# Kernel tuning notes

Hardware: AMD Instinct MI355X
Metric: run time of the kernel (lower is better)

Reference implementation:

```python
import jax, jax.numpy as jnp
import numpy as np

DILATED_K = 3  # init kwarg dilated_parameter_k -> 2**k = 8


def setup_inputs() -> dict:
    key = jax.random.key(0)
    k1, k2, k3, k4 = jax.random.split(key, 4)
    B, H, R, F = 16, 8, 400, 256
    A = jax.random.uniform(k1, (B, H, R, R), dtype=jnp.float32)
    feats = jax.random.normal(k2, (B, H, R, F), dtype=jnp.float32)
    # Linear(features, features) params (torch layout: weight [out, in], bias [out])
    lim = 1.0 / np.sqrt(F)
    W = jax.random.uniform(k3, (F, F), dtype=jnp.float32, minval=-lim, maxval=lim)
    b = jax.random.uniform(k4, (F,), dtype=jnp.float32, minval=-lim, maxval=lim)
    return {"Adjancy_Matrix": A, "features": feats, "W": W, "b": b}


def reference(Adjancy_Matrix, features, W, b):
    # Deterministic reference: takes the prob < 0.8 (dilated) branch of the
    # original module (the other branch is pure random dropout of the mask).
    two_k = 2 ** DILATED_K  # 8
    # torch.sort(A, descending=True, dim=3).indices == argsort of -A along last dim
    idx = jnp.argsort(-Adjancy_Matrix, axis=3)  # [B,H,R,R] int32
    # mask = 1 where sorted column index is 0 or in {2^k, ..., 2^k+4}
    mask = (idx == 0) | ((idx >= two_k) & (idx <= two_k + 4))
    R = Adjancy_Matrix.shape[2]
    mask = mask | jnp.eye(R, dtype=bool)  # add identity per (b, h), clamp >=1 -> 1
    masked_A = Adjancy_Matrix * mask.astype(Adjancy_Matrix.dtype)
    agg = jnp.einsum('bhij,bhjf->bhif', masked_A, features)  # [B,H,R,F]
    out = jax.nn.relu(agg @ W.T + b)
    return out + features
```

## Files before the change

### kernel.cpp

```cpp
#include <hip/hip_runtime.h>

typedef unsigned short u16;
typedef unsigned int   u32;
typedef __bf16 bf16x8 __attribute__((ext_vector_type(8)));
typedef float  f32x4  __attribute__((ext_vector_type(4)));
typedef u32    u32x4  __attribute__((ext_vector_type(4)));
typedef u16    u16x4  __attribute__((ext_vector_type(4)));
typedef u16    u16x8v __attribute__((ext_vector_type(8)));

#define R_DIM 400
#define F_DIM 256
#define M_TOT 51200
#define INVALID 0xFFFFFFFFu

__device__ __forceinline__ u16 f2bf(float f) {
    union { float f; u32 i; } x; x.f = f;
    u32 r = x.i + 0x7FFFu + ((x.i >> 16) & 1u);
    return (u16)(r >> 16);
}

__global__ __launch_bounds__(256) void wprep_f32(const float* __restrict__ W,
                                                 u16* __restrict__ Wf) {
    int g  = blockIdx.x * 256 + threadIdx.x;
    int ks = g >> 10;
    int T  = (g >> 6) & 15;
    int L  = g & 63;
    int n  = T * 16 + (L & 15);
    int k  = ks * 32 + (L >> 4) * 8;
    const float* wp = W + (size_t)n * F_DIM + k;
    float4 lo = *(const float4*)wp;
    float4 hi = *(const float4*)(wp + 4);
    u16x8v t;
    t[0] = f2bf(lo.x); t[1] = f2bf(lo.y); t[2] = f2bf(lo.z); t[3] = f2bf(lo.w);
    t[4] = f2bf(hi.x); t[5] = f2bf(hi.y); t[6] = f2bf(hi.z); t[7] = f2bf(hi.w);
    *(u16x8v*)(Wf + (size_t)g * 8) = t;
}

__global__ __launch_bounds__(256) void gcn_fused(const float* __restrict__ A,
                                                 const float* __restrict__ feats,
                                                 const u16*  __restrict__ Wf,
                                                 const float* __restrict__ bias,
                                                 float* __restrict__ out) {
    __shared__ __align__(16) u16 agg_lds[32][264];
    __shared__ __align__(16) u32 slot_lds[32][8];
    __shared__ __align__(16) u16 probeA[16][32];
    __shared__ __align__(16) u16 probeB[16][32];

    const int tid = threadIdx.x, wid = tid >> 6, lane = tid & 63;
    const int bid = (int)blockIdx.x;
    const int m0  = ((bid & 7) * 200 + (bid >> 3)) * 32;
    const int kg  = (lane >> 4) << 3;

    for (int e = tid; e < 512; e += 256) {
        int r = e >> 5, k = e & 31;
        probeA[r][k] = (k == 0) ? f2bf((float)r) : ((k == 1) ? f2bf(1.0f) : (u16)0);
        probeB[r][k] = (k == 0) ? f2bf(16.0f)    : ((k == 1) ? f2bf((float)r) : (u16)0);
    }

    const int rbase = wid * 8;

#pragma unroll 2
    for (int rr = 0; rr < 8; rr++) {
        const int r   = rbase + rr;
        const int row = m0 + r;
        const float* Ar = A + (size_t)row * R_DIM;

        float4 v0 = *(const float4*)(Ar + lane * 4);
        float4 v1 = *(const float4*)(Ar + (lane < 36 ? 256 + lane * 4 : 0));
        if (lane >= 36) { v1.x = -1.0f; v1.y = -1.0f; v1.z = -1.0f; v1.w = -1.0f; }

        float refs[6];
        refs[0] = __shfl(v0.x, 0);
        refs[1] = __shfl(v0.x, 2);
        refs[2] = __shfl(v0.y, 2);
        refs[3] = __shfl(v0.z, 2);
        refs[4] = __shfl(v0.w, 2);
        refs[5] = __shfl(v0.x, 3);
        const int cols[6] = {0, 8, 9, 10, 11, 12};

        int c[6] = {0, 0, 0, 0, 0, 0};
        float e0[4] = {v0.x, v0.y, v0.z, v0.w};
        float e1[4] = {v1.x, v1.y, v1.z, v1.w};
#pragma unroll
        for (int jj = 0; jj < 4; jj++) {
            float a = e0[jj]; int j = (lane << 2) + jj;
#pragma unroll
            for (int k = 0; k < 6; k++)
                c[k] += (a > refs[k] || (a == refs[k] && j < cols[k])) ? 1 : 0;
        }
#pragma unroll
        for (int jj = 0; jj < 4; jj++) {
            float a = e1[jj]; int j = 256 + (lane << 2) + jj;
#pragma unroll
            for (int k = 0; k < 6; k++)
                c[k] += (a > refs[k] || (a == refs[k] && j < cols[k])) ? 1 : 0;
        }
        u32 p0 = (u32)c[0] | ((u32)c[1] << 10) | ((u32)c[2] << 20);
        u32 p1 = (u32)c[3] | ((u32)c[4] << 10) | ((u32)c[5] << 20);
#pragma unroll
        for (int off = 32; off; off >>= 1) {
            p0 += __shfl_xor(p0, off);
            p1 += __shfl_xor(p1, off);
        }

        if (lane < 7) {
            u32 slot;
            if (lane < 6) {
                unsigned long long all = (((unsigned long long)p1) << 30) | (unsigned long long)p0;
                slot = (u32)((all >> (10 * lane)) & 1023u);
            } else {
                int i  = row % R_DIM;
                int q0 = p0 & 1023, q1 = (p0 >> 10) & 1023, q2 = (p0 >> 20) & 1023;
                int q3 = p1 & 1023, q4 = (p1 >> 10) & 1023, q5 = (p1 >> 20) & 1023;
                bool dup = (i == q0) | (i == q1) | (i == q2) | (i == q3) | (i == q4) | (i == q5);
                slot = dup ? INVALID : (u32)i;
            }
            slot_lds[r][lane] = slot;
        }
    }

    for (int rr = 0; rr < 8; rr++) {
        const int r   = rbase + rr;
        const int row = m0 + r;
        const int bh  = row / R_DIM;
        const float* Ar = A + (size_t)row * R_DIM;
        const float* fb = feats + (size_t)bh * R_DIM * F_DIM + lane * 4;

        u32 e[7];
#pragma unroll
        for (int s = 0; s < 7; s++) e[s] = slot_lds[r][s];

        float w[7]; float4 f[7];
#pragma unroll
        for (int s = 0; s < 7; s++) {
            u32 es = (e[s] == INVALID) ? 0u : e[s];
            w[s] = Ar[es];
            f[s] = *(const float4*)(fb + (size_t)es * F_DIM);
        }
        float a0 = 0.f, a1 = 0.f, a2 = 0.f, a3 = 0.f;
#pragma unroll
        for (int s = 0; s < 7; s++) {
            float ws = (e[s] == INVALID) ? 0.f : w[s];
            a0 += ws * f[s].x; a1 += ws * f[s].y; a2 += ws * f[s].z; a3 += ws * f[s].w;
        }
        u16x4 st = { f2bf(a0), f2bf(a1), f2bf(a2), f2bf(a3) };
        *(u16x4*)&agg_lds[r][lane * 4] = st;
    }
    __syncthreads();

    int rowi[4], coli[4];
    {
        bf16x8 pa = *(const bf16x8*)&probeA[lane & 15][kg];
        bf16x8 pb = *(const bf16x8*)&probeB[lane & 15][kg];
        f32x4 pd = {0.f, 0.f, 0.f, 0.f};
        pd = __builtin_amdgcn_mfma_f32_16x16x32_bf16(pa, pb, pd, 0, 0, 0);
#pragma unroll
        for (int reg = 0; reg < 4; reg++) {
            int v = (int)(pd[reg] + 0.5f);
            rowi[reg] = v >> 4;
            coli[reg] = v & 15;
        }
    }

    f32x4 acc[2][4];
#pragma unroll
    for (int mt = 0; mt < 2; mt++)
#pragma unroll
        for (int nt = 0; nt < 4; nt++)
            acc[mt][nt] = (f32x4){0.f, 0.f, 0.f, 0.f};

    for (int ks = 0; ks < 8; ks++) {
        bf16x8 af[2], bfr[4];
#pragma unroll
        for (int mt = 0; mt < 2; mt++)
            af[mt] = *(const bf16x8*)&agg_lds[mt * 16 + (lane & 15)][ks * 32 + kg];
#pragma unroll
        for (int nt = 0; nt < 4; nt++) {
            int T = wid * 4 + nt;
            u32x4 v = *(const u32x4*)(Wf + ((size_t)(ks * 16 + T) * 64 + lane) * 8);
            bfr[nt] = __builtin_bit_cast(bf16x8, v);
        }
#pragma unroll
        for (int mt = 0; mt < 2; mt++)
#pragma unroll
            for (int nt = 0; nt < 4; nt++)
                acc[mt][nt] = __builtin_amdgcn_mfma_f32_16x16x32_bf16(
                    af[mt], bfr[nt], acc[mt][nt], 0, 0, 0);
    }

#pragma unroll
    for (int nt = 0; nt < 4; nt++) {
        int nb = wid * 64 + nt * 16;
#pragma unroll
        for (int reg = 0; reg < 4; reg++) {
            int gn = nb + coli[reg];
            float bn = bias[gn];
#pragma unroll
            for (int mt = 0; mt < 2; mt++) {
                int gm = m0 + mt * 16 + rowi[reg];
                size_t off = (size_t)gm * F_DIM + gn;
                out[off] = fmaxf(acc[mt][nt][reg] + bn, 0.f) + feats[off];
            }
        }
    }
}

extern "C" void kernel_launch(void* const* d_in, const int* in_sizes, int n_in,
                              void* d_out, int out_size, void* d_ws, size_t ws_size,
                              hipStream_t stream) {
    const float* A     = (const float*)d_in[0];
    const float* feats = (const float*)d_in[1];
    const float* W     = (const float*)d_in[2];
    const float* bias  = (const float*)d_in[3];
    float* out = (float*)d_out;

    u16* Wf = (u16*)d_ws;

    wprep_f32<<<32, 256, 0, stream>>>(W, Wf);
    gcn_fused<<<M_TOT / 32, 256, 0, stream>>>(A, feats, Wf, bias, out);
}
```

Before: 219.8 us.

## Fuse slot selection with gather and software-pipeline A rows and feature loads

Merges the two per-row loops (rank counting and sparse gather) into one software-pipelined loop. The next A row is prefetched while the current one is ranked, and each row's feature gather overlaps the previous row's accumulate and store. Rank counting switches from per-lane counters plus a shuffle reduction to ballot and popcount, and the LDS slot staging is dropped. The cost is higher register pressure from holding two rows of gathered features, plus a serial chain of 48 ballots per row.

```diff
diff --git a/kernel.cpp b/kernel.cpp
--- a/kernel.cpp
+++ b/kernel.cpp
@@ -2,6 +2,7 @@
 
 typedef unsigned short u16;
 typedef unsigned int   u32;
+typedef unsigned long long u64;
 typedef __bf16 bf16x8 __attribute__((ext_vector_type(8)));
 typedef float  f32x4  __attribute__((ext_vector_type(4)));
 typedef u32    u32x4  __attribute__((ext_vector_type(4)));
@@ -11,7 +12,6 @@
 #define R_DIM 400
 #define F_DIM 256
 #define M_TOT 51200
-#define INVALID 0xFFFFFFFFu
 
 __device__ __forceinline__ u16 f2bf(float f) {
     union { float f; u32 i; } x; x.f = f;
@@ -36,13 +36,48 @@
     *(u16x8v*)(Wf + (size_t)g * 8) = t;
 }
 
+__device__ __forceinline__ void compute_slots(float4 v0, float4 v1r, int lane,
+                                              int row, u32 es[7], u32* dup_out) {
+    float4 v1 = v1r;
+    if (lane >= 36) { v1.x = -1.f; v1.y = -1.f; v1.z = -1.f; v1.w = -1.f; }
+    float refs[6];
+    refs[0] = __shfl(v0.x, 0);
+    refs[1] = __shfl(v0.x, 2);
+    refs[2] = __shfl(v0.y, 2);
+    refs[3] = __shfl(v0.z, 2);
+    refs[4] = __shfl(v0.w, 2);
+    refs[5] = __shfl(v0.x, 3);
+    const int cols[6] = {0, 8, 9, 10, 11, 12};
+    float e0[4] = {v0.x, v0.y, v0.z, v0.w};
+    float e1[4] = {v1.x, v1.y, v1.z, v1.w};
+    u32 cnt[6];
+#pragma unroll
+    for (int k = 0; k < 6; k++) {
+        int c = 0;
+#pragma unroll
+        for (int jj = 0; jj < 4; jj++) {
+            int j = (lane << 2) + jj;
+            c += __popcll(__ballot(e0[jj] > refs[k] ||
+                                   (e0[jj] == refs[k] && j < cols[k])));
+            c += __popcll(__ballot(e1[jj] > refs[k]));
+        }
+        cnt[k] = (u32)c;
+    }
+    int i = row % R_DIM;
+    bool dup = (i == (int)cnt[0]) | (i == (int)cnt[1]) | (i == (int)cnt[2]) |
+               (i == (int)cnt[3]) | (i == (int)cnt[4]) | (i == (int)cnt[5]);
+#pragma unroll
+    for (int s = 0; s < 6; s++) es[s] = cnt[s];
+    es[6] = (u32)i;
+    *dup_out = dup ? 1u : 0u;
+}
+
 __global__ __launch_bounds__(256) void gcn_fused(const float* __restrict__ A,
                                                  const float* __restrict__ feats,
                                                  const u16*  __restrict__ Wf,
                                                  const float* __restrict__ bias,
                                                  float* __restrict__ out) {
     __shared__ __align__(16) u16 agg_lds[32][264];
-    __shared__ __align__(16) u32 slot_lds[32][8];
     __shared__ __align__(16) u16 probeA[16][32];
     __shared__ __align__(16) u16 probeB[16][32];
 
@@ -59,92 +94,67 @@
 
     const int rbase = wid * 8;
 
-#pragma unroll 2
-    for (int rr = 0; rr < 8; rr++) {
-        const int r   = rbase + rr;
-        const int row = m0 + r;
-        const float* Ar = A + (size_t)row * R_DIM;
-
-        float4 v0 = *(const float4*)(Ar + lane * 4);
-        float4 v1 = *(const float4*)(Ar + (lane < 36 ? 256 + lane * 4 : 0));
-        if (lane >= 36) { v1.x = -1.0f; v1.y = -1.0f; v1.z = -1.0f; v1.w = -1.0f; }
-
-        float refs[6];
-        refs[0] = __shfl(v0.x, 0);
-        refs[1] = __shfl(v0.x, 2);
-        refs[2] = __shfl(v0.y, 2);
-        refs[3] = __shfl(v0.z, 2);
-        refs[4] = __shfl(v0.w, 2);
-        refs[5] = __shfl(v0.x, 3);
-        const int cols[6] = {0, 8, 9, 10, 11, 12};
-
-        int c[6] = {0, 0, 0, 0, 0, 0};
-        float e0[4] = {v0.x, v0.y, v0.z, v0.w};
-        float e1[4] = {v1.x, v1.y, v1.z, v1.w};
-#pragma unroll
-        for (int jj = 0; jj < 4; jj++) {
-            float a = e0[jj]; int j = (lane << 2) + jj;
-#pragma unroll
-            for (int k = 0; k < 6; k++)
-                c[k] += (a > refs[k] || (a == refs[k] && j < cols[k])) ? 1 : 0;
-        }
-#pragma unroll
-        for (int jj = 0; jj < 4; jj++) {
-            float a = e1[jj]; int j = 256 + (lane << 2) + jj;
-#pragma unroll
-            for (int k = 0; k < 6; k++)
-                c[k] += (a > refs[k] || (a == refs[k] && j < cols[k])) ? 1 : 0;
-        }
-        u32 p0 = (u32)c[0] | ((u32)c[1] << 10) | ((u32)c[2] << 20);
-        u32 p1 = (u32)c[3] | ((u32)c[4] << 10) | ((u32)c[5] << 20);
-#pragma unroll
-        for (int off = 32; off; off >>= 1) {
-            p0 += __shfl_xor(p0, off);
-            p1 += __shfl_xor(p1, off);
-        }
-
-        if (lane < 7) {
-            u32 slot;
-            if (lane < 6) {
-                unsigned long long all = (((unsigned long long)p1) << 30) | (unsigned long long)p0;
-                slot = (u32)((all >> (10 * lane)) & 1023u);
-            } else {
-                int i  = row % R_DIM;
-                int q0 = p0 & 1023, q1 = (p0 >> 10) & 1023, q2 = (p0 >> 20) & 1023;
-                int q3 = p1 & 1023, q4 = (p1 >> 10) & 1023, q5 = (p1 >> 20) & 1023;
-                bool dup = (i == q0) | (i == q1) | (i == q2) | (i == q3) | (i == q4) | (i == q5);
-                slot = dup ? INVALID : (u32)i;
-            }
-            slot_lds[r][lane] = slot;
-        }
-    }
-
-    for (int rr = 0; rr < 8; rr++) {
-        const int r   = rbase + rr;
-        const int row = m0 + r;
-        const int bh  = row / R_DIM;
-        const float* Ar = A + (size_t)row * R_DIM;
-        const float* fb = feats + (size_t)bh * R_DIM * F_DIM + lane * 4;
-
-        u32 e[7];
-#pragma unroll
-        for (int s = 0; s < 7; s++) e[s] = slot_lds[r][s];
-
-        float w[7]; float4 f[7];
-#pragma unroll
-        for (int s = 0; s < 7; s++) {
-            u32 es = (e[s] == INVALID) ? 0u : e[s];
-            w[s] = Ar[es];
-            f[s] = *(const float4*)(fb + (size_t)es * F_DIM);
-        }
-        float a0 = 0.f, a1 = 0.f, a2 = 0.f, a3 = 0.f;
-#pragma unroll
-        for (int s = 0; s < 7; s++) {
-            float ws = (e[s] == INVALID) ? 0.f : w[s];
-            a0 += ws * f[s].x; a1 += ws * f[s].y; a2 += ws * f[s].z; a3 += ws * f[s].w;
-        }
-        u16x4 st = { f2bf(a0), f2bf(a1), f2bf(a2), f2bf(a3) };
-        *(u16x4*)&agg_lds[r][lane * 4] = st;
+    {
+        const float* Ar0 = A + (size_t)(m0 + rbase) * R_DIM;
+        float4 pa0 = *(const float4*)(Ar0 + lane * 4);
+        float4 pa1 = *(const float4*)(Ar0 + (lane < 36 ? 256 + lane * 4 : 0));
+
+        float  w_p[7];
+        float4 f_p[7];
+        u32    dup_p = 0;
+
+#pragma unroll
+        for (int rr = 0; rr < 8; rr++) {
+            const int r   = rbase + rr;
+            const int row = m0 + r;
+            float4 v0 = pa0, v1 = pa1;
+            if (rr < 7) {
+                const float* An = A + (size_t)(row + 1) * R_DIM;
+                pa0 = *(const float4*)(An + lane * 4);
+                pa1 = *(const float4*)(An + (lane < 36 ? 256 + lane * 4 : 0));
+            }
+
+            u32 es[7], dupm;
+            compute_slots(v0, v1, lane, row, es, &dupm);
+
+            const int bh = row / R_DIM;
+            const float* Ar = A + (size_t)row * R_DIM;
+            const float* fb = feats + (size_t)bh * R_DIM * F_DIM + lane * 4;
+
+            float w[7]; float4 f[7];
+#pragma unroll
+            for (int s = 0; s < 7; s++) {
+                u32 e = es[s];
+                w[s] = Ar[e];
+                f[s] = *(const float4*)(fb + (size_t)e * F_DIM);
+            }
+
+            if (rr > 0) {
+                float a0 = 0.f, a1 = 0.f, a2 = 0.f, a3 = 0.f;
+#pragma unroll
+                for (int s = 0; s < 7; s++) {
+                    float ws = (s == 6 && dup_p) ? 0.f : w_p[s];
+                    a0 += ws * f_p[s].x; a1 += ws * f_p[s].y;
+                    a2 += ws * f_p[s].z; a3 += ws * f_p[s].w;
+                }
+                u16x4 st = { f2bf(a0), f2bf(a1), f2bf(a2), f2bf(a3) };
+                *(u16x4*)&agg_lds[r - 1][lane * 4] = st;
+            }
+#pragma unroll
+            for (int s = 0; s < 7; s++) { w_p[s] = w[s]; f_p[s] = f[s]; }
+            dup_p = dupm;
+        }
+        {
+            float a0 = 0.f, a1 = 0.f, a2 = 0.f, a3 = 0.f;
+#pragma unroll
+            for (int s = 0; s < 7; s++) {
+                float ws = (s == 6 && dup_p) ? 0.f : w_p[s];
+                a0 += ws * f_p[s].x; a1 += ws * f_p[s].y;
+                a2 += ws * f_p[s].z; a3 += ws * f_p[s].w;
+            }
+            u16x4 st = { f2bf(a0), f2bf(a1), f2bf(a2), f2bf(a3) };
+            *(u16x4*)&agg_lds[rbase + 7][lane * 4] = st;
+        }
     }
     __syncthreads();
 
```

Result: faster. 215.3 us (-2.0%).
